# Kernel optimization log

Measured on AMD Instinct MI355X. Metric: run time of the kernel, lower is better.

The kernel has to match this reference:

```python
import jax, jax.numpy as jnp
import numpy as np

B, T, I, H, NL, HORIZON, NQ = 256, 512, 64, 512, 2, 30, 3
MEDIAN_IDX = 1  # quantiles.index(0.5)


def _lstm_cell(xt, h, c, Wih, Whh, b):
    # PyTorch gate order: i, f, g, o
    g = xt @ Wih.T + h @ Whh.T + b
    i, f, gg, o = jnp.split(g, 4, axis=-1)
    c_new = jax.nn.sigmoid(f) * c + jax.nn.sigmoid(i) * jnp.tanh(gg)
    h_new = jax.nn.sigmoid(o) * jnp.tanh(c_new)
    return h_new, c_new


def _run_lstm_layer(xs, Wih, Whh, b):
    # xs: [T, B, in]; zero initial state (torch default)
    batch = xs.shape[1]
    hidden = Whh.shape[1]
    h0 = jnp.zeros((batch, hidden), xs.dtype)

    def step(carry, xt):
        h, c = carry
        h, c = _lstm_cell(xt, h, c, Wih, Whh, b)
        return (h, c), h

    (hT, cT), hs = jax.lax.scan(step, (h0, h0), xs)
    return hs, hT, cT


def setup_inputs() -> dict:
    key = jax.random.key(0)
    ks = jax.random.split(key, 24)
    k = 1.0 / np.sqrt(H)

    def u(kk, shape):
        return jax.random.uniform(kk, shape, jnp.float32, -k, k)

    inp = {
        "x": jax.random.normal(ks[0], (B, T, I), jnp.float32),
        # encoder layer 0 (input I) and layer 1 (input H)
        "enc_Wih0": u(ks[1], (4 * H, I)),
        "enc_Whh0": u(ks[2], (4 * H, H)),
        "enc_bih0": u(ks[3], (4 * H,)),
        "enc_bhh0": u(ks[4], (4 * H,)),
        "enc_Wih1": u(ks[5], (4 * H, H)),
        "enc_Whh1": u(ks[6], (4 * H, H)),
        "enc_bih1": u(ks[7], (4 * H,)),
        "enc_bhh1": u(ks[8], (4 * H,)),
        # decoder layer 0 (input H+1) and layer 1 (input H)
        "dec_Wih0": u(ks[9], (4 * H, H + 1)),
        "dec_Whh0": u(ks[10], (4 * H, H)),
        "dec_bih0": u(ks[11], (4 * H,)),
        "dec_bhh0": u(ks[12], (4 * H,)),
        "dec_Wih1": u(ks[13], (4 * H, H)),
        "dec_Whh1": u(ks[14], (4 * H, H)),
        "dec_bih1": u(ks[15], (4 * H,)),
        "dec_bhh1": u(ks[16], (4 * H,)),
        # attention: W [H,H] (no bias), V [H] (Linear(H,1) weight)
        "attn_W": u(ks[17], (H, H)),
        "attn_v": u(ks[18], (H,)),
        # output projection [NQ, H] + bias
        "out_W": u(ks[19], (NQ, H)),
        "out_b": u(ks[20], (NQ,)),
    }
    return inp


def reference(x, enc_Wih0, enc_Whh0, enc_bih0, enc_bhh0,
              enc_Wih1, enc_Whh1, enc_bih1, enc_bhh1,
              dec_Wih0, dec_Whh0, dec_bih0, dec_bhh0,
              dec_Wih1, dec_Whh1, dec_bih1, dec_bhh1,
              attn_W, attn_v, out_W, out_b):
    # ---- encoder: 2-layer LSTM over time (eval mode: no dropout) ----
    xs = jnp.transpose(x, (1, 0, 2))  # [T, B, I]
    hs0, _, _ = _run_lstm_layer(xs, enc_Wih0, enc_Whh0, enc_bih0 + enc_bhh0)
    hs1, h_last, c_last = _run_lstm_layer(hs0, enc_Wih1, enc_Whh1, enc_bih1 + enc_bhh1)
    encoder_outputs = jnp.transpose(hs1, (1, 0, 2))  # [B, T, H]

    # precompute W(encoder_outputs) once (same math as per-step recompute)
    enc_proj = jnp.einsum('bth,gh->btg', encoder_outputs, attn_W)  # [B, T, H]

    b_dec0 = dec_bih0 + dec_bhh0
    b_dec1 = dec_bih1 + dec_bhh1

    dec_input0 = x[:, -1, 0:1]  # [B, 1]

    def step(carry, _):
        h, c, inp = carry
        # Bahdanau attention
        dec_proj = h @ attn_W.T  # [B, H]
        energies = jnp.einsum('bth,h->bt', jnp.tanh(enc_proj + dec_proj[:, None, :]), attn_v)
        attn = jax.nn.softmax(energies, axis=1)  # [B, T]
        ctx = jnp.einsum('bt,bth->bh', attn, encoder_outputs)  # [B, H]
        # decoder LSTM, 1 timestep; both layers restart from the SAME (h, c)
        # (the module repeats the last layer's state across layers each step)
        x0 = jnp.concatenate([inp, ctx], axis=1)  # [B, H+1]
        h0, c0 = _lstm_cell(x0, h, c, dec_Wih0, dec_Whh0, b_dec0)
        h1, c1 = _lstm_cell(h0, h, c, dec_Wih1, dec_Whh1, b_dec1)
        out = h1 @ out_W.T + out_b  # [B, NQ]
        new_inp = out[:, MEDIAN_IDX:MEDIAN_IDX + 1]  # feed back median quantile
        return (h1, c1, new_inp), out

    _, preds = jax.lax.scan(step, (h_last, c_last, dec_input0), None, length=HORIZON)
    return jnp.transpose(preds, (1, 0, 2))  # [B, HORIZON, NQ]
```

## Files before the change

### kernel.cpp

```cpp
#include <hip/hip_runtime.h>


typedef _Float16 half_t;
typedef __attribute__((ext_vector_type(8)))  _Float16 f16x8;
typedef __attribute__((ext_vector_type(16))) float    f32x16;

#define MFMA(a,b,c) __builtin_amdgcn_mfma_f32_32x32x16_f16((a),(b),(c),0,0,0)
#define CBAR()      asm volatile("" ::: "memory")
#define AUXC 17

template<int N> __device__ __forceinline__ void waitvm() {
  asm volatile("s_waitcnt vmcnt(%0)" :: "n"(N) : "memory");
}

__device__ __forceinline__ float fsig(float x)  { return 1.0f / (1.0f + __expf(-x)); }
__device__ __forceinline__ float ftanh(float x) { return 1.0f - 2.0f / (1.0f + __expf(2.0f * x)); }

union FU { float f; unsigned u; };
union HU { _Float16 h; unsigned short u; };
__device__ __forceinline__ float ldfa(const float* p) {
  unsigned v = __hip_atomic_load((const unsigned*)p, __ATOMIC_RELAXED, __HIP_MEMORY_SCOPE_AGENT);
  FU c; c.u = v; return c.f;
}
__device__ __forceinline__ void stfa(float* p, float v) {
  FU c; c.f = v;
  __hip_atomic_store((unsigned*)p, c.u, __ATOMIC_RELAXED, __HIP_MEMORY_SCOPE_AGENT);
}
__device__ __forceinline__ void stha(half_t* p, float v) {
  HU c; c.h = (half_t)v;
  __hip_atomic_store((unsigned short*)p, c.u, __ATOMIC_RELAXED, __HIP_MEMORY_SCOPE_AGENT);
}
__device__ __forceinline__ void st64(float* p, float a, float b) {
  FU x, y; x.f = a; y.f = b;
  unsigned long long v = (unsigned long long)x.u | ((unsigned long long)y.u << 32);
  __hip_atomic_store((unsigned long long*)p, v, __ATOMIC_RELAXED, __HIP_MEMORY_SCOPE_AGENT);
}
__device__ __forceinline__ void ld64(const float* p, float& a, float& b) {
  unsigned long long v = __hip_atomic_load((const unsigned long long*)p, __ATOMIC_RELAXED, __HIP_MEMORY_SCOPE_AGENT);
  FU x, y; x.u = (unsigned)v; y.u = (unsigned)(v >> 32); a = x.f; b = y.f;
}

static constexpr size_t O_X16 = 0;
static constexpr size_t O_WL0 = O_X16 + (size_t)512*256*128*2;
static constexpr size_t O_WL1 = O_WL0 + (size_t)2048*640*2;
static constexpr size_t O_WP1 = O_WL1 + (size_t)2048*1024*2;
static constexpr size_t O_WD0 = O_WP1 + (size_t)4672*512*2;
static constexpr size_t O_WD1 = O_WD0 + (size_t)2048*512*2;
static constexpr size_t O_BL0 = O_WD1 + (size_t)2048*512*2;
static constexpr size_t O_BL1 = O_BL0 + 8192;
static constexpr size_t O_BD0 = O_BL1 + 8192;
static constexpr size_t O_BD1 = O_BD0 + 8192;
static constexpr size_t O_W0C = O_BD1 + 8192;
static constexpr size_t O_H0B = O_W0C + 8192;
static constexpr size_t O_H1B = O_H0B + (size_t)2*256*512*2;
static constexpr size_t O_HD1 = O_H1B + (size_t)2*256*512*2;
static constexpr size_t O_H0D = O_HD1 + (size_t)256*512*2;
static constexpr size_t O_CTX = O_H0D + (size_t)256*512*2;
static constexpr size_t O_C0  = O_CTX + (size_t)256*512*2;
static constexpr size_t O_C1  = O_C0  + (size_t)256*512*4;
static constexpr size_t O_INP = O_C1  + (size_t)256*512*4;
static constexpr size_t O_GAT = O_INP + 1024;
static constexpr size_t O_EO  = O_GAT + (size_t)256*4672*4;
static constexpr size_t O_EP  = O_EO  + (size_t)256*512*512*2;
static constexpr size_t WS_NEED = O_EP + (size_t)256*512*512*2;

__device__ __align__(4096) unsigned char g_ws[WS_NEED];
__device__ int g_bar[2048];
__device__ int g_flags[1024];

#define WSH(o) ((half_t*)(g_ws + (o)))
#define WSCH(o) ((const half_t*)(g_ws + (o)))
#define WSF(o) ((float*)(g_ws + (o)))
#define WSCF(o) ((const float*)(g_ws + (o)))
#define BLINE(i) (g_bar + ((size_t)(i) << 5))

__device__ __forceinline__ int gperm(int n) { return (n & 3) * 512 + (n >> 2); }

__device__ __forceinline__ void gbarf(int g, int r, int step) {
  __syncthreads();
  if (threadIdx.x < 64) {
    if (threadIdx.x == 0)
      __hip_atomic_store(&g_flags[(g << 6) + r], step,
                         __ATOMIC_RELAXED, __HIP_MEMORY_SCOPE_AGENT);
    const int* fp = &g_flags[(g << 6) + threadIdx.x];
    for (;;) {
      int v = __hip_atomic_load(fp, __ATOMIC_RELAXED, __HIP_MEMORY_SCOPE_AGENT);
      if (__all(v >= step)) break;
      __builtin_amdgcn_s_sleep(1);
    }
  }
  __syncthreads();
}

__device__ __forceinline__ void gbar_acq(int g, int sub) {
  __syncthreads();
  if (threadIdx.x == 0) {
    int* cnt = BLINE(g * 2 + sub);
    int* mst = BLINE(8 + g);
    int* gs  = BLINE(12 + g * 2 + sub);
    int old = __hip_atomic_load(gs, __ATOMIC_RELAXED, __HIP_MEMORY_SCOPE_AGENT);
    int a = __hip_atomic_fetch_add(cnt, 1, __ATOMIC_ACQ_REL, __HIP_MEMORY_SCOPE_AGENT);
    if (a == 31) {
      __hip_atomic_store(cnt, 0, __ATOMIC_RELAXED, __HIP_MEMORY_SCOPE_AGENT);
      int m = __hip_atomic_fetch_add(mst, 1, __ATOMIC_ACQ_REL, __HIP_MEMORY_SCOPE_AGENT);
      if (m == 1) {
        __hip_atomic_store(mst, 0, __ATOMIC_RELAXED, __HIP_MEMORY_SCOPE_AGENT);
        __hip_atomic_fetch_add(BLINE(12 + g * 2), 1, __ATOMIC_RELEASE, __HIP_MEMORY_SCOPE_AGENT);
        __hip_atomic_fetch_add(BLINE(12 + g * 2 + 1), 1, __ATOMIC_RELEASE, __HIP_MEMORY_SCOPE_AGENT);
      }
    }
    while (__hip_atomic_load(gs, __ATOMIC_RELAXED, __HIP_MEMORY_SCOPE_AGENT) == old)
      __builtin_amdgcn_s_sleep(2);
    (void)__hip_atomic_load(gs, __ATOMIC_ACQUIRE, __HIP_MEMORY_SCOPE_AGENT);
  }
  __syncthreads();
}

struct Seg { const half_t* p; int stride; int row0; };

template<int AXA, int AXB>
__device__ __forceinline__ void stageA(Seg sa, Seg sb, int cSplit, int c,
                                       int lane, int wid, char* dst) {
  bool isA = c < cSplit;
  Seg s = isA ? sa : sb;
  int kb = (isA ? c : (c - cSplit)) * 128;
  const half_t* g = s.p + (size_t)(s.row0 + (lane & 31)) * s.stride
                        + kb + (wid << 4) + ((lane >> 5) << 3);
  if (isA) {
    __builtin_amdgcn_global_load_lds(
        (const __attribute__((address_space(1))) unsigned int*)g,
        (__attribute__((address_space(3))) unsigned int*)dst, 16, 0, AXA);
    __builtin_amdgcn_global_load_lds(
        (const __attribute__((address_space(1))) unsigned int*)(g + (size_t)32 * s.stride),
        (__attribute__((address_space(3))) unsigned int*)(dst + 1024), 16, 0, AXA);
  } else {
    __builtin_amdgcn_global_load_lds(
        (const __attribute__((address_space(1))) unsigned int*)g,
        (__attribute__((address_space(3))) unsigned int*)dst, 16, 0, AXB);
    __builtin_amdgcn_global_load_lds(
        (const __attribute__((address_space(1))) unsigned int*)(g + (size_t)32 * s.stride),
        (__attribute__((address_space(3))) unsigned int*)(dst + 1024), 16, 0, AXB);
  }
}

template<int C, int NC, int CSPLIT, int AXA, int AXB>
__device__ __forceinline__ void kreg(Seg sa, Seg sb,
                                     const f16x8 (&B0)[8], const f16x8 (&B1)[8],
                                     int lane, int wid, char* asg, f32x16 acc[2][2]) {
  if constexpr (C < NC) {
    constexpr int rem = NC - 1 - C;
    waitvm<2 * (rem < 3 ? rem : 3)>();
    char* ab = asg + (size_t)(((C & 3) * 8 + wid)) * 2048 + lane * 16;
    f16x8 a0 = *(const f16x8*)ab;
    f16x8 a1 = *(const f16x8*)(ab + 1024);
    acc[0][0] = MFMA(a0, B0[C], acc[0][0]);
    acc[0][1] = MFMA(a0, B1[C], acc[0][1]);
    acc[1][0] = MFMA(a1, B0[C], acc[1][0]);
    acc[1][1] = MFMA(a1, B1[C], acc[1][1]);
    if constexpr (C + 4 < NC)
      stageA<AXA, AXB>(sa, sb, CSPLIT, C + 4, lane, wid,
                       asg + (size_t)((((C + 4) & 3) * 8 + wid)) * 2048);
    CBAR();
    kreg<C + 1, NC, CSPLIT, AXA, AXB>(sa, sb, B0, B1, lane, wid, asg, acc);
  }
}

template<int NC, int CSPLIT, int AXA, int AXB>
__device__ __forceinline__ void gemm_regB(Seg sa, Seg sb,
                                          const f16x8 (&B0)[8], const f16x8 (&B1)[8],
                                          int lane, int wid, char* asg, f32x16 acc[2][2]) {
  #pragma unroll
  for (int c = 0; c < (NC < 4 ? NC : 4); c++) {
    stageA<AXA, AXB>(sa, sb, CSPLIT, c, lane, wid, asg + (size_t)((c & 3) * 8 + wid) * 2048);
    CBAR();
  }
  kreg<0, NC, CSPLIT, AXA, AXB>(sa, sb, B0, B1, lane, wid, asg, acc);
}

template<int C, int NC>
__device__ __forceinline__ void kks(int lane, int wid, char* asg, f32x16 acc[2][2],
                                    f16x8 (&b0)[4], f16x8 (&b1)[4]) {
  if constexpr (C < NC) {
    waitvm<4 * (NC - 1 - C)>();
    char* ab = asg + (size_t)(C * 8 + wid) * 2048 + lane * 16;
    f16x8 a0 = *(const f16x8*)ab;
    f16x8 a1 = *(const f16x8*)(ab + 1024);
    acc[0][0] = MFMA(a0, b0[C], acc[0][0]);
    acc[0][1] = MFMA(a0, b1[C], acc[0][1]);
    acc[1][0] = MFMA(a1, b0[C], acc[1][0]);
    acc[1][1] = MFMA(a1, b1[C], acc[1][1]);
    CBAR();
    kks<C + 1, NC>(lane, wid, asg, acc, b0, b1);
  }
}

template<int NC, int AXA, int AXB>
__device__ __forceinline__ void gemm_ks(Seg sa, Seg sb, int cSplit, const half_t* Wt,
                                        int lane, int wid, char* asg, f32x16 acc[2][2]) {
  const half_t* wb = Wt + (wid << 1) * 512 + lane * 8;
  f16x8 b0[4], b1[4];
  #pragma unroll
  for (int c = 0; c < NC; c++) {
    stageA<AXA, AXB>(sa, sb, cSplit, c, lane, wid, asg + (size_t)(c * 8 + wid) * 2048);
    CBAR();
    b0[c] = *(const f16x8*)(wb + (size_t)c * 8192);
    b1[c] = *(const f16x8*)(wb + (size_t)c * 8192 + 512);
    CBAR();
  }
  kks<0, NC>(lane, wid, asg, acc, b0, b1);
}

__device__ __forceinline__ void acc_wr(float* dst, int lane, f32x16 acc[2][2]) {
  #pragma unroll
  for (int t = 0; t < 4; t++) {
    f32x16 a = acc[t >> 1][t & 1];
    #pragma unroll
    for (int r4 = 0; r4 < 4; r4++)
      *(float4*)(dst + ((t * 4 + r4) * 64 + lane) * 4) =
          make_float4(a[r4*4], a[r4*4+1], a[r4*4+2], a[r4*4+3]);
  }
}
__device__ __forceinline__ void acc_add(const float* src, int lane, f32x16 acc[2][2]) {
  #pragma unroll
  for (int t = 0; t < 4; t++) {
    #pragma unroll
    for (int r4 = 0; r4 < 4; r4++) {
      float4 v = *(const float4*)(src + ((t * 4 + r4) * 64 + lane) * 4);
      acc[t>>1][t&1][r4*4]   += v.x;
      acc[t>>1][t&1][r4*4+1] += v.y;
      acc[t>>1][t&1][r4*4+2] += v.z;
      acc[t>>1][t&1][r4*4+3] += v.w;
    }
  }
}
__device__ __forceinline__ void reduce8(f32x16 acc[2][2], float* red, int lane, int wid) {
  if (wid >= 4) acc_wr(red + (size_t)(wid - 4) * 4096, lane, acc);
  __syncthreads();
  if (wid < 4) acc_add(red + (size_t)wid * 4096, lane, acc);
  if (wid == 2 || wid == 3) acc_wr(red + (size_t)wid * 4096, lane, acc);
  __syncthreads();
  if (wid < 2) {
    acc_add(red + (size_t)(wid + 2) * 4096, lane, acc);
    float* zone = red + 8192 + (size_t)wid * 4096;
    #pragma unroll
    for (int ms = 0; ms < 2; ms++)
      #pragma unroll
      for (int ns = 0; ns < 2; ns++)
        #pragma unroll
        for (int rr = 0; rr < 16; rr++) {
          int row = ms * 32 + (rr & 3) + ((rr >> 2) << 3) + ((lane >> 5) << 2);
          zone[row * 64 + ns * 32 + (lane & 31)] = acc[ms][ns][rr];
        }
  }
  __syncthreads();
}
__device__ __forceinline__ float4 rsum4(const float* red, int row, int col) {
  float4 a = *(const float4*)&red[8192 + row * 64 + col];
  float4 b = *(const float4*)&red[12288 + row * 64 + col];
  return make_float4(a.x + b.x, a.y + b.y, a.z + b.z, a.w + b.w);
}

__global__ void __launch_bounds__(512, 2) kmain(const float* __restrict__ attn_v,
                                                const float* __restrict__ out_b,
                                                float* __restrict__ out) {
  __shared__ __align__(16) char asg[65536];
  __shared__ float red[16384];

  const half_t* x16 = WSCH(O_X16);
  const half_t* wL0 = WSCH(O_WL0);
  const half_t* wL1 = WSCH(O_WL1);
  const half_t* wP1 = WSCH(O_WP1);
  const half_t* wD0 = WSCH(O_WD0);
  const half_t* wD1 = WSCH(O_WD1);
  half_t* h0bB = WSH(O_H0B);
  half_t* h1bB = WSH(O_H1B);
  half_t* hd1  = WSH(O_HD1);
  half_t* h0d  = WSH(O_H0D);
  half_t* ctx  = WSH(O_CTX);
  half_t* eo   = WSH(O_EO);
  half_t* ep   = WSH(O_EP);
  float* c1 = WSF(O_C1);
  float* inp = WSF(O_INP);
  float* gates = WSF(O_GAT);

  const int tid = threadIdx.x;
  const int wid = tid >> 6;
  const int lane = tid & 63;
  const int g = blockIdx.x & 3;
  const int r = blockIdx.x >> 2;
  const int sub = r & 1;
  const int m0 = g << 6;
  const f32x16 zv = {0,0,0,0,0,0,0,0,0,0,0,0,0,0,0,0};
  int bstep = 0;

  {
    const bool isL1 = r >= 32;
    const int n0 = (r & 31) << 6;

    const half_t* wbase = isL1 ? (wL1 + (size_t)(n0 >> 6) * (8 * 8192))
                               : (wL0 + (size_t)(n0 >> 6) * (5 * 8192));
    const half_t* wb = wbase + (wid << 1) * 512 + lane * 8;
    const int ncB = isL1 ? 8 : 5;
    f16x8 B0[8], B1[8];
    #pragma unroll
    for (int c = 0; c < 8; c++) {
      if (c < ncB) {
        B0[c] = *(const f16x8*)(wb + (size_t)c * 8192);
        B1[c] = *(const f16x8*)(wb + (size_t)c * 8192 + 512);
      }
    }
    const int eu = tid & 15;
    const int ebl = tid >> 4;
    const float* bias = isL1 ? WSCF(O_BL1) : WSCF(O_BL0);
    float4 breg = *(const float4*)&bias[n0 + eu * 4];
    float creg0 = 0.f, creg1 = 0.f;

    for (int s = 0; s <= 512; s++) {
      const bool active = isL1 ? (s > 0) : (s < 512);
      if (active) {
        const half_t* h0r = h0bB + (size_t)((s + 1) & 1) * (256 * 512);
        f32x16 acc[2][2] = {{zv, zv}, {zv, zv}};
        int t;
        if (!isL1) {
          t = s;
          gemm_regB<5, 1, 0, AUXC>(Seg{x16, 128, t * 256 + m0}, Seg{h0r, 512, m0},
                                   B0, B1, lane, wid, asg, acc);
        } else {
          t = s - 1;
          const half_t* h1r = h1bB + (size_t)(s & 1) * (256 * 512);
          gemm_regB<8, 4, AUXC, AUXC>(Seg{h0r, 512, m0}, Seg{h1r, 512, m0},
                                      B0, B1, lane, wid, asg, acc);
        }
        reduce8(acc, red, lane, wid);
        half_t* hb = isL1 ? (h1bB + (size_t)((s - 1) & 1) * (256 * 512))
                          : (h0bB + (size_t)(s & 1) * (256 * 512));
        #pragma unroll
        for (int it = 0; it < 2; it++) {
          int bl = ebl + it * 32;
          float4 g4 = rsum4(red, bl, eu * 4);
          float gi = g4.x + breg.x, gf = g4.y + breg.y;
          float gz = g4.z + breg.z, go = g4.w + breg.w;
          float cold = it ? creg1 : creg0;
          float cn = fsig(gf) * cold + fsig(gi) * ftanh(gz);
          float hn = fsig(go) * ftanh(cn);
          if (it) creg1 = cn; else creg0 = cn;
          int bg = m0 + bl, ug = (n0 >> 2) + eu;
          stha(&hb[bg * 512 + ug], hn);
          if (isL1) eo[((size_t)bg * 512 + t) * 512 + ug] = (half_t)hn;
        }
      }
      gbarf(g, r, ++bstep);
    }

    if (isL1) {
      int ug = (n0 >> 2) + eu;
      c1[(m0 + ebl) * 512 + ug] = creg0;
      c1[(m0 + ebl + 32) * 512 + ug] = creg1;
    }
  }
  gbar_acq(g, sub);

  for (int j = 0; j < 64; j++) {
    const int jj = r * 64 + j;
    const int ml = jj >> 3;
    const int nt = jj & 7;
    const int row0 = (g << 15) + ml * 64;
    f32x16 acc[2][2] = {{zv, zv}, {zv, zv}};
    gemm_ks<4, 0, 0>(Seg{eo, 512, row0}, Seg{eo, 512, row0}, 4,
                     wP1 + (size_t)nt * (4 * 8192), lane, wid, asg, acc);
    reduce8(acc, red, lane, wid);
    {
      int row = tid >> 3, col = (tid & 7) * 8;
      float4 a0 = rsum4(red, row, col);
      float4 a1 = rsum4(red, row, col + 4);
      f16x8 h8;
      h8[0] = (half_t)a0.x; h8[1] = (half_t)a0.y; h8[2] = (half_t)a0.z; h8[3] = (half_t)a0.w;
      h8[4] = (half_t)a1.x; h8[5] = (half_t)a1.y; h8[6] = (half_t)a1.z; h8[7] = (half_t)a1.w;
      *(f16x8*)&ep[(size_t)(row0 + row) * 512 + nt * 64 + col] = h8;
    }
    __syncthreads();
  }
  gbar_acq(g, sub);

  for (int d = 0; d <= 30; d++) {
    const half_t* hs = (d == 0) ? (h1bB + 256 * 512) : hd1;
    for (int jj = r; jj < 73; jj += 64) {
      const int n0p = jj * 64;
      f32x16 acc[2][2] = {{zv, zv}, {zv, zv}};
      gemm_ks<4, AUXC, AUXC>(Seg{hs, 512, m0}, Seg{hs, 512, m0}, 4,
                             wP1 + (size_t)jj * (4 * 8192), lane, wid, asg, acc);
      reduce8(acc, red, lane, wid);
      if (n0p < 4608) {
        #pragma unroll
        for (int it = 0; it < 2; it++) {
          int q = it * 512 + tid;
          int row = q >> 4, col = (q & 15) * 4;
          float4 v4 = rsum4(red, row, col);
          float* dst = &gates[(size_t)(m0 + row) * 4672 + n0p + col];
          st64(dst, v4.x, v4.y);
          st64(dst + 2, v4.z, v4.w);
        }
      } else if (d > 0) {
        if (tid < 64) {
          int bg = m0 + tid;
          float v0 = red[8192 + tid * 64 + 0] + red[12288 + tid * 64 + 0] + out_b[0];
          float v1 = red[8192 + tid * 64 + 1] + red[12288 + tid * 64 + 1] + out_b[1];
          float v2 = red[8192 + tid * 64 + 2] + red[12288 + tid * 64 + 2] + out_b[2];
          out[(size_t)bg * 90 + (d - 1) * 3 + 0] = v0;
          out[(size_t)bg * 90 + (d - 1) * 3 + 1] = v1;
          out[(size_t)bg * 90 + (d - 1) * 3 + 2] = v2;
          stfa(&inp[bg], v1);
        }
      }
      __syncthreads();
    }
    gbarf(g, r, ++bstep);
    if (d == 30) break;

    {
      const int b = m0 + r;
      float* dpb = red;
      float* vb  = red + 512;
      float* eb  = red + 1024;
      float* ab2 = red + 2048;
      float* sc  = red + 2560;
      float* pm  = red + 4096;
      dpb[tid] = ldfa(&gates[(size_t)b * 4672 + tid]);
      vb[tid]  = attn_v[tid];
      __syncthreads();
      float va[8], da[8];
      {
        float4 t0 = *(const float4*)&vb[lane * 8];
        float4 t1 = *(const float4*)&vb[lane * 8 + 4];
        float4 t2 = *(const float4*)&dpb[lane * 8];
        float4 t3 = *(const float4*)&dpb[lane * 8 + 4];
        va[0]=t0.x; va[1]=t0.y; va[2]=t0.z; va[3]=t0.w;
        va[4]=t1.x; va[5]=t1.y; va[6]=t1.z; va[7]=t1.w;
        da[0]=t2.x; da[1]=t2.y; da[2]=t2.z; da[3]=t2.w;
        da[4]=t3.x; da[5]=t3.y; da[6]=t3.z; da[7]=t3.w;
      }
      const half_t* eprow = ep + ((size_t)b << 18) + (size_t)(wid * 64) * 512 + lane * 8;
      for (int tt = 0; tt < 64; tt++) {
        f16x8 e8 = *(const f16x8*)(eprow + (size_t)tt * 512);
        float sum = 0.f;
        #pragma unroll
        for (int jq = 0; jq < 8; jq++)
          sum += va[jq] * ftanh((float)e8[jq] + da[jq]);
        #pragma unroll
        for (int off = 32; off > 0; off >>= 1) sum += __shfl_down(sum, off, 64);
        if (lane == 0) eb[wid * 64 + tt] = sum;
      }
      __syncthreads();
      float e0 = eb[tid];
      float mx = e0;
      #pragma unroll
      for (int off = 32; off > 0; off >>= 1) mx = fmaxf(mx, __shfl_xor(mx, off, 64));
      if (lane == 0) sc[wid] = mx;
      __syncthreads();
      mx = sc[0];
      #pragma unroll
      for (int q = 1; q < 8; q++) mx = fmaxf(mx, sc[q]);
      float x0 = __expf(e0 - mx);
      float ssum = x0;
      #pragma unroll
      for (int off = 32; off > 0; off >>= 1) ssum += __shfl_xor(ssum, off, 64);
      __syncthreads();
      if (lane == 0) sc[8 + wid] = ssum;
      __syncthreads();
      float tot = sc[8];
      #pragma unroll
      for (int q = 1; q < 8; q++) tot += sc[8 + q];
      float inv = 1.f / tot;
      ab2[tid] = x0 * inv;
      __syncthreads();
      float pacc[8] = {0,0,0,0,0,0,0,0};
      const half_t* eow = eo + ((size_t)b << 18) + (size_t)(wid * 64) * 512 + lane * 8;
      for (int tt = 0; tt < 64; tt++) {
        f16x8 h8 = *(const f16x8*)(eow + (size_t)tt * 512);
        float at = ab2[wid * 64 + tt];
        #pragma unroll
        for (int jq = 0; jq < 8; jq++) pacc[jq] += at * (float)h8[jq];
      }
      #pragma unroll
      for (int jq = 0; jq < 8; jq++) pm[wid * 512 + lane * 8 + jq] = pacc[jq];
      __syncthreads();
      float sctx = 0.f;
      #pragma unroll
      for (int w = 0; w < 8; w++) sctx += pm[w * 512 + tid];
      stha(&ctx[(b << 9) + tid], sctx);
    }
    gbarf(g, r, ++bstep);

    if (r < 32) {
      const int n0 = r << 6;
      f32x16 acc[2][2] = {{zv, zv}, {zv, zv}};
      gemm_ks<4, AUXC, AUXC>(Seg{ctx, 512, m0}, Seg{ctx, 512, m0}, 4,
                             wD0 + (size_t)(n0 >> 6) * (4 * 8192), lane, wid, asg, acc);
      reduce8(acc, red, lane, wid);
      const float* bD0 = WSCF(O_BD0);
      const float* w0c = WSCF(O_W0C);
      #pragma unroll
      for (int it = 0; it < 2; it++) {
        int q = it * 512 + tid;
        int u = q & 15, bl = q >> 4;
        int bg = m0 + bl, ug = (n0 >> 2) + u, nl = n0 + u * 4;
        float4 g4 = rsum4(red, bl, u * 4);
        float p0, p1, p2, p3;
        ld64(&gates[(size_t)bg * 4672 + 512 + nl], p0, p1);
        ld64(&gates[(size_t)bg * 4672 + 512 + nl + 2], p2, p3);
        float4 b4 = *(const float4*)&bD0[nl];
        float4 w4 = *(const float4*)&w0c[nl];
        float iv = ldfa(&inp[bg]);
        float gi = g4.x + p0 + b4.x + iv * w4.x;
        float gf = g4.y + p1 + b4.y + iv * w4.y;
        float gz = g4.z + p2 + b4.z + iv * w4.z;
        float go = g4.w + p3 + b4.w + iv * w4.w;
        float cold = c1[bg * 512 + ug];
        float cn = fsig(gf) * cold + fsig(gi) * ftanh(gz);
        stha(&h0d[bg * 512 + ug], fsig(go) * ftanh(cn));
      }
    }
    gbarf(g, r, ++bstep);

    if (r < 32) {
      const int n0 = r << 6;
      f32x16 acc[2][2] = {{zv, zv}, {zv, zv}};
      gemm_ks<4, AUXC, AUXC>(Seg{h0d, 512, m0}, Seg{h0d, 512, m0}, 4,
                             wD1 + (size_t)(n0 >> 6) * (4 * 8192), lane, wid, asg, acc);
      reduce8(acc, red, lane, wid);
      const float* bD1 = WSCF(O_BD1);
      #pragma unroll
      for (int it = 0; it < 2; it++) {
        int q = it * 512 + tid;
        int u = q & 15, bl = q >> 4;
        int bg = m0 + bl, ug = (n0 >> 2) + u, nl = n0 + u * 4;
        float4 g4 = rsum4(red, bl, u * 4);
        float p0, p1, p2, p3;
        ld64(&gates[(size_t)bg * 4672 + 2560 + nl], p0, p1);
        ld64(&gates[(size_t)bg * 4672 + 2560 + nl + 2], p2, p3);
        float4 b4 = *(const float4*)&bD1[nl];
        float gi = g4.x + p0 + b4.x;
        float gf = g4.y + p1 + b4.y;
        float gz = g4.z + p2 + b4.z;
        float go = g4.w + p3 + b4.w;
        float cold = c1[bg * 512 + ug];
        float cn = fsig(gf) * cold + fsig(gi) * ftanh(gz);
        float hn = fsig(go) * ftanh(cn);
        c1[bg * 512 + ug] = cn;
        stha(&hd1[bg * 512 + ug], hn);
      }
    }
    gbarf(g, r, ++bstep);
  }
}

__global__ void kpackB(size_t dstOff, int id, int Ntiles, int NC,
                       const float* s0, const float* s1,
                       const float* s2, const float* s3) {
  half_t* dst = (half_t*)(g_ws + dstOff);
  size_t total = (size_t)Ntiles * NC * 8192;
  size_t i = (size_t)blockIdx.x * 256 + threadIdx.x;
  size_t stride = (size_t)gridDim.x * 256;
  for (size_t e = i; e < total; e += stride) {
    int j = e & 7;
    int l = (e >> 3) & 63;
    int bh = (e >> 9) & 1;
    int w = (e >> 10) & 7;
    int tc = (int)(e >> 13);
    int c = tc % NC;
    int tile = tc / NC;
    int n = tile * 64 + bh * 32 + (l & 31);
    int k = c * 128 + w * 16 + ((l >> 5) << 3) + j;
    float v = 0.f;
    if (id == 0) {
      int pn = gperm(n);
      if (k < 64) v = s0[(size_t)pn * 64 + k];
      else if (k >= 128) v = s1[(size_t)pn * 512 + (k - 128)];
    } else if (id == 1) {
      int pn = gperm(n);
      v = (k < 512) ? s0[(size_t)pn * 512 + k] : s1[(size_t)pn * 512 + (k - 512)];
    } else if (id == 2) {
      if (n < 512) v = s0[((size_t)n << 9) + k];
      else if (n < 2560) v = s1[((size_t)gperm(n - 512) << 9) + k];
      else if (n < 4608) v = s2[((size_t)gperm(n - 2560) << 9) + k];
      else if (n < 4611) v = s3[((size_t)(n - 4608) << 9) + k];
    } else if (id == 3) {
      v = s0[(size_t)gperm(n) * 513 + 1 + k];
    } else {
      v = s0[((size_t)gperm(n) << 9) + k];
    }
    dst[e] = (half_t)v;
  }
}

__global__ void kmisc(const float* ebih0, const float* ebhh0, const float* ebih1, const float* ebhh1,
                      const float* dbih0, const float* dbhh0, const float* dbih1, const float* dbhh1,
                      const float* dWih0, const float* x) {
  float* bL0 = WSF(O_BL0);
  float* bL1 = WSF(O_BL1);
  float* bD0 = WSF(O_BD0);
  float* bD1 = WSF(O_BD1);
  float* w0c = WSF(O_W0C);
  half_t* h0b = WSH(O_H0B);
  half_t* h1b = WSH(O_H1B);
  float* c1 = WSF(O_C1);
  float* inp = WSF(O_INP);
  int i = blockIdx.x * 256 + threadIdx.x, stride = gridDim.x * 256;
  for (int idx = i; idx < 262144; idx += stride) {
    if (idx < 2048) {
      int pn = gperm(idx);
      bL0[idx] = ebih0[pn] + ebhh0[pn];
      bL1[idx] = ebih1[pn] + ebhh1[pn];
      bD0[idx] = dbih0[pn] + dbhh0[pn];
      bD1[idx] = dbih1[pn] + dbhh1[pn];
      w0c[idx] = dWih0[(size_t)pn * 513];
      g_bar[idx] = 0;
    }
    if (idx < 1024) g_flags[idx] = 0;
    if (idx < 256) inp[idx] = x[((size_t)idx * 512 + 511) * 64];
    h0b[idx] = (half_t)0.f;
    h1b[idx] = (half_t)0.f;
    if (idx < 131072) c1[idx] = 0.f;
  }
}

__global__ void kx16(const float* x) {
  half_t* dst = WSH(O_X16);
  size_t i = (size_t)blockIdx.x * 256 + threadIdx.x;
  size_t stride = (size_t)gridDim.x * 256;
  for (size_t e = i; e < (size_t)512 * 256 * 128; e += stride) {
    int t = (int)(e >> 15);
    int b = (int)((e >> 7) & 255);
    int ii = (int)(e & 127);
    dst[e] = (ii < 64) ? (half_t)x[((size_t)b * 512 + t) * 64 + ii] : (half_t)0.f;
  }
}

extern "C" void kernel_launch(void* const* d_in, const int* in_sizes, int n_in,
                              void* d_out, int out_size, void* d_ws, size_t ws_size,
                              hipStream_t stream) {
  const float* x     = (const float*)d_in[0];
  const float* eWih0 = (const float*)d_in[1];
  const float* eWhh0 = (const float*)d_in[2];
  const float* ebih0 = (const float*)d_in[3];
  const float* ebhh0 = (const float*)d_in[4];
  const float* eWih1 = (const float*)d_in[5];
  const float* eWhh1 = (const float*)d_in[6];
  const float* ebih1 = (const float*)d_in[7];
  const float* ebhh1 = (const float*)d_in[8];
  const float* dWih0 = (const float*)d_in[9];
  const float* dWhh0 = (const float*)d_in[10];
  const float* dbih0 = (const float*)d_in[11];
  const float* dbhh0 = (const float*)d_in[12];
  const float* dWih1 = (const float*)d_in[13];
  const float* dWhh1 = (const float*)d_in[14];
  const float* dbih1 = (const float*)d_in[15];
  const float* dbhh1 = (const float*)d_in[16];
  const float* attnW = (const float*)d_in[17];
  const float* attnv = (const float*)d_in[18];
  const float* outW  = (const float*)d_in[19];
  const float* outb  = (const float*)d_in[20];
  (void)in_sizes; (void)n_in; (void)out_size; (void)d_ws; (void)ws_size;

  kpackB<<<1024, 256, 0, stream>>>(O_WL0, 0, 32, 5, eWih0, eWhh0, nullptr, nullptr);
  kpackB<<<1024, 256, 0, stream>>>(O_WL1, 1, 32, 8, eWih1, eWhh1, nullptr, nullptr);
  kpackB<<<1024, 256, 0, stream>>>(O_WP1, 2, 73, 4, attnW, dWhh0, dWhh1, outW);
  kpackB<<<1024, 256, 0, stream>>>(O_WD0, 3, 32, 4, dWih0, nullptr, nullptr, nullptr);
  kpackB<<<1024, 256, 0, stream>>>(O_WD1, 4, 32, 4, dWih1, nullptr, nullptr, nullptr);
  kmisc<<<1024, 256, 0, stream>>>(ebih0, ebhh0, ebih1, ebhh1,
                                  dbih0, dbhh0, dbih1, dbhh1, dWih0, x);
  kx16<<<2048, 256, 0, stream>>>(x);

  float* outp = (float*)d_out;
  void* args[] = {(void*)&attnv, (void*)&outb, (void*)&outp};
  hipError_t e = hipLaunchCooperativeKernel((void*)kmain, dim3(256), dim3(512),
                                            args, 0, stream);
  if (e != hipSuccess) {
    kmain<<<dim3(256), dim3(512), 0, stream>>>(attnv, outb, outp);
  }
}
```

Before: 8.513 ms.

## Repartition persistent LSTM kernel into 8 XCC-local groups with fused encoder layers

```diff
diff --git a/kernel.cpp b/kernel.cpp
--- a/kernel.cpp
+++ b/kernel.cpp
@@ -7,7 +7,6 @@
 
 #define MFMA(a,b,c) __builtin_amdgcn_mfma_f32_32x32x16_f16((a),(b),(c),0,0,0)
 #define CBAR()      asm volatile("" ::: "memory")
-#define AUXC 17
 
 template<int N> __device__ __forceinline__ void waitvm() {
   asm volatile("s_waitcnt vmcnt(%0)" :: "n"(N) : "memory");
@@ -18,25 +17,53 @@
 
 union FU { float f; unsigned u; };
 union HU { _Float16 h; unsigned short u; };
+
+template<bool FAST>
 __device__ __forceinline__ float ldfa(const float* p) {
-  unsigned v = __hip_atomic_load((const unsigned*)p, __ATOMIC_RELAXED, __HIP_MEMORY_SCOPE_AGENT);
-  FU c; c.u = v; return c.f;
-}
+  if constexpr (FAST) {
+    float v;
+    asm volatile("global_load_dword %0, %1, off sc0\n\ts_waitcnt vmcnt(0)"
+                 : "=v"(v) : "v"(p) : "memory");
+    return v;
+  } else {
+    unsigned v = __hip_atomic_load((const unsigned*)p, __ATOMIC_RELAXED, __HIP_MEMORY_SCOPE_AGENT);
+    FU c; c.u = v; return c.f;
+  }
+}
+template<bool FAST>
 __device__ __forceinline__ void stfa(float* p, float v) {
   FU c; c.f = v;
-  __hip_atomic_store((unsigned*)p, c.u, __ATOMIC_RELAXED, __HIP_MEMORY_SCOPE_AGENT);
-}
+  if constexpr (FAST)
+    asm volatile("global_store_dword %0, %1, off sc0" :: "v"(p), "v"(c.u) : "memory");
+  else
+    __hip_atomic_store((unsigned*)p, c.u, __ATOMIC_RELAXED, __HIP_MEMORY_SCOPE_AGENT);
+}
+template<bool FAST>
 __device__ __forceinline__ void stha(half_t* p, float v) {
   HU c; c.h = (half_t)v;
-  __hip_atomic_store((unsigned short*)p, c.u, __ATOMIC_RELAXED, __HIP_MEMORY_SCOPE_AGENT);
-}
+  if constexpr (FAST)
+    asm volatile("global_store_short %0, %1, off sc0" :: "v"(p), "v"((unsigned)c.u) : "memory");
+  else
+    __hip_atomic_store((unsigned short*)p, c.u, __ATOMIC_RELAXED, __HIP_MEMORY_SCOPE_AGENT);
+}
+template<bool FAST>
 __device__ __forceinline__ void st64(float* p, float a, float b) {
   FU x, y; x.f = a; y.f = b;
   unsigned long long v = (unsigned long long)x.u | ((unsigned long long)y.u << 32);
-  __hip_atomic_store((unsigned long long*)p, v, __ATOMIC_RELAXED, __HIP_MEMORY_SCOPE_AGENT);
-}
+  if constexpr (FAST)
+    asm volatile("global_store_dwordx2 %0, %1, off sc0" :: "v"(p), "v"(v) : "memory");
+  else
+    __hip_atomic_store((unsigned long long*)p, v, __ATOMIC_RELAXED, __HIP_MEMORY_SCOPE_AGENT);
+}
+template<bool FAST>
 __device__ __forceinline__ void ld64(const float* p, float& a, float& b) {
-  unsigned long long v = __hip_atomic_load((const unsigned long long*)p, __ATOMIC_RELAXED, __HIP_MEMORY_SCOPE_AGENT);
+  unsigned long long v;
+  if constexpr (FAST) {
+    asm volatile("global_load_dwordx2 %0, %1, off sc0\n\ts_waitcnt vmcnt(0)"
+                 : "=v"(v) : "v"(p) : "memory");
+  } else {
+    v = __hip_atomic_load((const unsigned long long*)p, __ATOMIC_RELAXED, __HIP_MEMORY_SCOPE_AGENT);
+  }
   FU x, y; x.u = (unsigned)v; y.u = (unsigned)(v >> 32); a = x.f; b = y.f;
 }
 
@@ -67,6 +94,7 @@
 __device__ __align__(4096) unsigned char g_ws[WS_NEED];
 __device__ int g_bar[2048];
 __device__ int g_flags[1024];
+__device__ int g_xcc[256];
 
 #define WSH(o) ((half_t*)(g_ws + (o)))
 #define WSCH(o) ((const half_t*)(g_ws + (o)))
@@ -80,9 +108,9 @@
   __syncthreads();
   if (threadIdx.x < 64) {
     if (threadIdx.x == 0)
-      __hip_atomic_store(&g_flags[(g << 6) + r], step,
+      __hip_atomic_store(&g_flags[(g << 5) + r], step,
                          __ATOMIC_RELAXED, __HIP_MEMORY_SCOPE_AGENT);
-    const int* fp = &g_flags[(g << 6) + threadIdx.x];
+    const int* fp = &g_flags[(g << 5) + (threadIdx.x & 31)];
     for (;;) {
       int v = __hip_atomic_load(fp, __ATOMIC_RELAXED, __HIP_MEMORY_SCOPE_AGENT);
       if (__all(v >= step)) break;
@@ -92,21 +120,22 @@
   __syncthreads();
 }
 
-__device__ __forceinline__ void gbar_acq(int g, int sub) {
+__device__ __forceinline__ void gbar_acq8() {
   __syncthreads();
   if (threadIdx.x == 0) {
-    int* cnt = BLINE(g * 2 + sub);
-    int* mst = BLINE(8 + g);
-    int* gs  = BLINE(12 + g * 2 + sub);
+    const int g = blockIdx.x & 7;
+    int* cnt = BLINE(g);
+    int* mst = BLINE(8);
+    int* gs  = BLINE(16 + g);
     int old = __hip_atomic_load(gs, __ATOMIC_RELAXED, __HIP_MEMORY_SCOPE_AGENT);
     int a = __hip_atomic_fetch_add(cnt, 1, __ATOMIC_ACQ_REL, __HIP_MEMORY_SCOPE_AGENT);
     if (a == 31) {
       __hip_atomic_store(cnt, 0, __ATOMIC_RELAXED, __HIP_MEMORY_SCOPE_AGENT);
       int m = __hip_atomic_fetch_add(mst, 1, __ATOMIC_ACQ_REL, __HIP_MEMORY_SCOPE_AGENT);
-      if (m == 1) {
+      if (m == 7) {
         __hip_atomic_store(mst, 0, __ATOMIC_RELAXED, __HIP_MEMORY_SCOPE_AGENT);
-        __hip_atomic_fetch_add(BLINE(12 + g * 2), 1, __ATOMIC_RELEASE, __HIP_MEMORY_SCOPE_AGENT);
-        __hip_atomic_fetch_add(BLINE(12 + g * 2 + 1), 1, __ATOMIC_RELEASE, __HIP_MEMORY_SCOPE_AGENT);
+        for (int q = 0; q < 8; q++)
+          __hip_atomic_fetch_add(BLINE(16 + q), 1, __ATOMIC_RELEASE, __HIP_MEMORY_SCOPE_AGENT);
       }
     }
     while (__hip_atomic_load(gs, __ATOMIC_RELAXED, __HIP_MEMORY_SCOPE_AGENT) == old)
@@ -114,6 +143,13 @@
     (void)__hip_atomic_load(gs, __ATOMIC_ACQUIRE, __HIP_MEMORY_SCOPE_AGENT);
   }
   __syncthreads();
+}
+
+template<int AX>
+__device__ __forceinline__ void gld(const half_t* gp, char* lp) {
+  __builtin_amdgcn_global_load_lds(
+      (const __attribute__((address_space(1))) unsigned int*)gp,
+      (__attribute__((address_space(3))) unsigned int*)lp, 16, 0, AX);
 }
 
 struct Seg { const half_t* p; int stride; int row0; };
@@ -124,57 +160,15 @@
   bool isA = c < cSplit;
   Seg s = isA ? sa : sb;
   int kb = (isA ? c : (c - cSplit)) * 128;
-  const half_t* g = s.p + (size_t)(s.row0 + (lane & 31)) * s.stride
-                        + kb + (wid << 4) + ((lane >> 5) << 3);
+  const half_t* gp = s.p + (size_t)(s.row0 + (lane & 31)) * s.stride
+                         + kb + (wid << 4) + ((lane >> 5) << 3);
   if (isA) {
-    __builtin_amdgcn_global_load_lds(
-        (const __attribute__((address_space(1))) unsigned int*)g,
-        (__attribute__((address_space(3))) unsigned int*)dst, 16, 0, AXA);
-    __builtin_amdgcn_global_load_lds(
-        (const __attribute__((address_space(1))) unsigned int*)(g + (size_t)32 * s.stride),
-        (__attribute__((address_space(3))) unsigned int*)(dst + 1024), 16, 0, AXA);
+    gld<AXA>(gp, dst);
+    gld<AXA>(gp + (size_t)32 * s.stride, dst + 1024);
   } else {
-    __builtin_amdgcn_global_load_lds(
-        (const __attribute__((address_space(1))) unsigned int*)g,
-        (__attribute__((address_space(3))) unsigned int*)dst, 16, 0, AXB);
-    __builtin_amdgcn_global_load_lds(
-        (const __attribute__((address_space(1))) unsigned int*)(g + (size_t)32 * s.stride),
-        (__attribute__((address_space(3))) unsigned int*)(dst + 1024), 16, 0, AXB);
-  }
-}
-
-template<int C, int NC, int CSPLIT, int AXA, int AXB>
-__device__ __forceinline__ void kreg(Seg sa, Seg sb,
-                                     const f16x8 (&B0)[8], const f16x8 (&B1)[8],
-                                     int lane, int wid, char* asg, f32x16 acc[2][2]) {
-  if constexpr (C < NC) {
-    constexpr int rem = NC - 1 - C;
-    waitvm<2 * (rem < 3 ? rem : 3)>();
-    char* ab = asg + (size_t)(((C & 3) * 8 + wid)) * 2048 + lane * 16;
-    f16x8 a0 = *(const f16x8*)ab;
-    f16x8 a1 = *(const f16x8*)(ab + 1024);
-    acc[0][0] = MFMA(a0, B0[C], acc[0][0]);
-    acc[0][1] = MFMA(a0, B1[C], acc[0][1]);
-    acc[1][0] = MFMA(a1, B0[C], acc[1][0]);
-    acc[1][1] = MFMA(a1, B1[C], acc[1][1]);
-    if constexpr (C + 4 < NC)
-      stageA<AXA, AXB>(sa, sb, CSPLIT, C + 4, lane, wid,
-                       asg + (size_t)((((C + 4) & 3) * 8 + wid)) * 2048);
-    CBAR();
-    kreg<C + 1, NC, CSPLIT, AXA, AXB>(sa, sb, B0, B1, lane, wid, asg, acc);
-  }
-}
-
-template<int NC, int CSPLIT, int AXA, int AXB>
-__device__ __forceinline__ void gemm_regB(Seg sa, Seg sb,
-                                          const f16x8 (&B0)[8], const f16x8 (&B1)[8],
-                                          int lane, int wid, char* asg, f32x16 acc[2][2]) {
-  #pragma unroll
-  for (int c = 0; c < (NC < 4 ? NC : 4); c++) {
-    stageA<AXA, AXB>(sa, sb, CSPLIT, c, lane, wid, asg + (size_t)((c & 3) * 8 + wid) * 2048);
-    CBAR();
-  }
-  kreg<0, NC, CSPLIT, AXA, AXB>(sa, sb, B0, B1, lane, wid, asg, acc);
+    gld<AXB>(gp, dst);
+    gld<AXB>(gp + (size_t)32 * s.stride, dst + 1024);
+  }
 }
 
 template<int C, int NC>
@@ -208,6 +202,61 @@
     CBAR();
   }
   kks<0, NC>(lane, wid, asg, acc, b0, b1);
+}
+
+template<int C, int NC>
+__device__ __forceinline__ void kks32(char* wslr, f32x16 (&acc)[2][2],
+                                      f16x8 (&b0)[4], f16x8 (&b1)[4]) {
+  if constexpr (C < NC) {
+    waitvm<3 * (NC - 1 - C) + 2>();
+    f16x8 a = *(const f16x8*)(wslr + C * 8192);
+    acc[0][0] = MFMA(a, b0[C], acc[0][0]);
+    acc[0][1] = MFMA(a, b1[C], acc[0][1]);
+    CBAR();
+    kks32<C + 1, NC>(wslr, acc, b0, b1);
+  }
+}
+
+template<int NC, int AX>
+__device__ __forceinline__ void gemm_ks32(const half_t* aP, const half_t* Wt,
+                                          int lane, int wid, char* asg, f32x16 (&acc)[2][2]) {
+  char* wsl = asg + wid * 1024;
+  const half_t* wb = Wt + (wid << 1) * 512 + lane * 8;
+  f16x8 b0[4], b1[4];
+  #pragma unroll
+  for (int c = 0; c < NC; c++) {
+    gld<AX>(aP + c * 128, wsl + c * 8192);
+    CBAR();
+    b0[c] = *(const f16x8*)(wb + (size_t)c * 8192);
+    b1[c] = *(const f16x8*)(wb + (size_t)c * 8192 + 512);
+    CBAR();
+  }
+  kks32<0, NC>(wsl + lane * 16, acc, b0, b1);
+}
+
+template<int C>
+__device__ __forceinline__ void encL0(const char* wslr, const f16x8 (&B0)[5],
+                                      const f16x8 (&B1)[5], f32x16 (&acc)[2][2]) {
+  if constexpr (C < 5) {
+    waitvm<8 - C>();
+    f16x8 a = *(const f16x8*)(wslr + C * 8192);
+    acc[0][0] = MFMA(a, B0[C], acc[0][0]);
+    acc[0][1] = MFMA(a, B1[C], acc[0][1]);
+    CBAR();
+    encL0<C + 1>(wslr, B0, B1, acc);
+  }
+}
+template<int C>
+__device__ __forceinline__ void encL1(const char* wslr, const f16x8 (&B0)[8],
+                                      const f16x8 (&B1)[8], f32x16 (&acc)[2][2]) {
+  if constexpr (C < 8) {
+    if constexpr (C >= 4) waitvm<7 - C>();
+    f16x8 a = *(const f16x8*)(wslr + (C + 1) * 8192);
+    acc[1][0] = MFMA(a, B0[C], acc[1][0]);
+    acc[1][1] = MFMA(a, B1[C], acc[1][1]);
+    CBAR();
+    encL1<C + 1>(wslr, B0, B1, acc);
+  }
 }
 
 __device__ __forceinline__ void acc_wr(float* dst, int lane, f32x16 acc[2][2]) {
@@ -260,11 +309,12 @@
   return make_float4(a.x + b.x, a.y + b.y, a.z + b.z, a.w + b.w);
 }
 
-__global__ void __launch_bounds__(512, 2) kmain(const float* __restrict__ attn_v,
-                                                const float* __restrict__ out_b,
-                                                float* __restrict__ out) {
-  __shared__ __align__(16) char asg[65536];
-  __shared__ float red[16384];
+template<bool FAST>
+__device__ __noinline__ void run_all(int g, int r, const float* attn_v,
+                                     const float* out_b, float* out,
+                                     char* asg, float* red) {
+  constexpr int AXH = FAST ? 1 : 17;
+  constexpr size_t PP = (size_t)256 * 512;
 
   const half_t* x16 = WSCH(O_X16);
   const half_t* wL0 = WSCH(O_WL0);
@@ -286,85 +336,80 @@
   const int tid = threadIdx.x;
   const int wid = tid >> 6;
   const int lane = tid & 63;
-  const int g = blockIdx.x & 3;
-  const int r = blockIdx.x >> 2;
-  const int sub = r & 1;
-  const int m0 = g << 6;
+  const int m0 = g << 5;
   const f32x16 zv = {0,0,0,0,0,0,0,0,0,0,0,0,0,0,0,0};
   int bstep = 0;
 
+  const int koff = (wid << 4) + ((lane >> 5) << 3);
+  const size_t aofs = (size_t)(m0 + (lane & 31)) * 512 + koff;
+  const size_t xofs = (size_t)(m0 + (lane & 31)) * 128 + koff;
+  char* wsl = asg + wid * 1024;
+  const char* wslr = wsl + lane * 16;
+
   {
-    const bool isL1 = r >= 32;
-    const int n0 = (r & 31) << 6;
-
-    const half_t* wbase = isL1 ? (wL1 + (size_t)(n0 >> 6) * (8 * 8192))
-                               : (wL0 + (size_t)(n0 >> 6) * (5 * 8192));
-    const half_t* wb = wbase + (wid << 1) * 512 + lane * 8;
-    const int ncB = isL1 ? 8 : 5;
-    f16x8 B0[8], B1[8];
+    const int n0 = r << 6;
+    const half_t* wb0 = wL0 + (size_t)r * (5 * 8192) + (wid << 1) * 512 + lane * 8;
+    const half_t* wb1 = wL1 + (size_t)r * (8 * 8192) + (wid << 1) * 512 + lane * 8;
+    f16x8 B0L0[5], B1L0[5], B0L1[8], B1L1[8];
+    #pragma unroll
+    for (int c = 0; c < 5; c++) {
+      B0L0[c] = *(const f16x8*)(wb0 + (size_t)c * 8192);
+      B1L0[c] = *(const f16x8*)(wb0 + (size_t)c * 8192 + 512);
+    }
     #pragma unroll
     for (int c = 0; c < 8; c++) {
-      if (c < ncB) {
-        B0[c] = *(const f16x8*)(wb + (size_t)c * 8192);
-        B1[c] = *(const f16x8*)(wb + (size_t)c * 8192 + 512);
+      B0L1[c] = *(const f16x8*)(wb1 + (size_t)c * 8192);
+      B1L1[c] = *(const f16x8*)(wb1 + (size_t)c * 8192 + 512);
+    }
+    const int eu = tid & 15, ebl = tid >> 4;
+    const float4 breg0 = *(const float4*)&(WSCF(O_BL0))[n0 + eu * 4];
+    const float4 breg1 = *(const float4*)&(WSCF(O_BL1))[n0 + eu * 4];
+    const int bg = m0 + ebl, ug = (r << 4) + eu;
+    float creg0 = 0.f, creg1 = 0.f;
+
+    for (int s = 0; s <= 512; s++) {
+      {
+        const int tc = s < 512 ? s : 511;
+        const half_t* xp  = x16 + (((size_t)tc) << 15) + xofs;
+        const half_t* h0p = h0bB + (size_t)((s + 1) & 1) * PP + aofs;
+        const half_t* h1p = h1bB + (size_t)(s & 1) * PP + aofs;
+        gld<0>(xp, wsl);
+        #pragma unroll
+        for (int c = 0; c < 4; c++) gld<AXH>(h0p + c * 128, wsl + (c + 1) * 8192);
+        #pragma unroll
+        for (int c = 0; c < 4; c++) gld<AXH>(h1p + c * 128, wsl + (c + 5) * 8192);
+        CBAR();
       }
-    }
-    const int eu = tid & 15;
-    const int ebl = tid >> 4;
-    const float* bias = isL1 ? WSCF(O_BL1) : WSCF(O_BL0);
-    float4 breg = *(const float4*)&bias[n0 + eu * 4];
-    float creg0 = 0.f, creg1 = 0.f;
-
-    for (int s = 0; s <= 512; s++) {
-      const bool active = isL1 ? (s > 0) : (s < 512);
-      if (active) {
-        const half_t* h0r = h0bB + (size_t)((s + 1) & 1) * (256 * 512);
-        f32x16 acc[2][2] = {{zv, zv}, {zv, zv}};
-        int t;
-        if (!isL1) {
-          t = s;
-          gemm_regB<5, 1, 0, AUXC>(Seg{x16, 128, t * 256 + m0}, Seg{h0r, 512, m0},
-                                   B0, B1, lane, wid, asg, acc);
-        } else {
-          t = s - 1;
-          const half_t* h1r = h1bB + (size_t)(s & 1) * (256 * 512);
-          gemm_regB<8, 4, AUXC, AUXC>(Seg{h0r, 512, m0}, Seg{h1r, 512, m0},
-                                      B0, B1, lane, wid, asg, acc);
-        }
-        reduce8(acc, red, lane, wid);
-        half_t* hb = isL1 ? (h1bB + (size_t)((s - 1) & 1) * (256 * 512))
-                          : (h0bB + (size_t)(s & 1) * (256 * 512));
-        #pragma unroll
-        for (int it = 0; it < 2; it++) {
-          int bl = ebl + it * 32;
-          float4 g4 = rsum4(red, bl, eu * 4);
-          float gi = g4.x + breg.x, gf = g4.y + breg.y;
-          float gz = g4.z + breg.z, go = g4.w + breg.w;
-          float cold = it ? creg1 : creg0;
-          float cn = fsig(gf) * cold + fsig(gi) * ftanh(gz);
-          float hn = fsig(go) * ftanh(cn);
-          if (it) creg1 = cn; else creg0 = cn;
-          int bg = m0 + bl, ug = (n0 >> 2) + eu;
-          stha(&hb[bg * 512 + ug], hn);
-          if (isL1) eo[((size_t)bg * 512 + t) * 512 + ug] = (half_t)hn;
-        }
+      f32x16 acc[2][2] = {{zv, zv}, {zv, zv}};
+      encL0<0>(wslr, B0L0, B1L0, acc);
+      encL1<0>(wslr, B0L1, B1L1, acc);
+      reduce8(acc, red, lane, wid);
+      if (s < 512) {
+        float4 g4 = rsum4(red, ebl, eu * 4);
+        float cn = fsig(g4.y + breg0.y) * creg0 + fsig(g4.x + breg0.x) * ftanh(g4.z + breg0.z);
+        float hn = fsig(g4.w + breg0.w) * ftanh(cn);
+        creg0 = cn;
+        stha<FAST>(&h0bB[(size_t)(s & 1) * PP + (size_t)bg * 512 + ug], hn);
+      }
+      if (s > 0) {
+        float4 g4 = rsum4(red, ebl + 32, eu * 4);
+        float cn = fsig(g4.y + breg1.y) * creg1 + fsig(g4.x + breg1.x) * ftanh(g4.z + breg1.z);
+        float hn = fsig(g4.w + breg1.w) * ftanh(cn);
+        creg1 = cn;
+        stha<FAST>(&h1bB[(size_t)((s + 1) & 1) * PP + (size_t)bg * 512 + ug], hn);
+        eo[((size_t)bg * 512 + (s - 1)) * 512 + ug] = (half_t)hn;
       }
       gbarf(g, r, ++bstep);
     }
-
-    if (isL1) {
-      int ug = (n0 >> 2) + eu;
-      c1[(m0 + ebl) * 512 + ug] = creg0;
-      c1[(m0 + ebl + 32) * 512 + ug] = creg1;
-    }
-  }
-  gbar_acq(g, sub);
+    c1[(size_t)bg * 512 + ug] = creg1;
+  }
+  gbar_acq8();
 
   for (int j = 0; j < 64; j++) {
-    const int jj = r * 64 + j;
+    const int jj = (r << 6) + j;
     const int ml = jj >> 3;
     const int nt = jj & 7;
-    const int row0 = (g << 15) + ml * 64;
+    const int row0 = (g << 14) + ml * 64;
     f32x16 acc[2][2] = {{zv, zv}, {zv, zv}};
     gemm_ks<4, 0, 0>(Seg{eo, 512, row0}, Seg{eo, 512, row0}, 4,
                      wP1 + (size_t)nt * (4 * 8192), lane, wid, asg, acc);
@@ -380,28 +425,24 @@
     }
     __syncthreads();
   }
-  gbar_acq(g, sub);
+  gbar_acq8();
 
   for (int d = 0; d <= 30; d++) {
-    const half_t* hs = (d == 0) ? (h1bB + 256 * 512) : hd1;
-    for (int jj = r; jj < 73; jj += 64) {
-      const int n0p = jj * 64;
+    const half_t* hs = (d == 0) ? (h1bB + PP) : hd1;
+
+    for (int jj = r; jj < 73; jj += 32) {
+      if (d == 30 && jj != 72) continue;
       f32x16 acc[2][2] = {{zv, zv}, {zv, zv}};
-      gemm_ks<4, AUXC, AUXC>(Seg{hs, 512, m0}, Seg{hs, 512, m0}, 4,
-                             wP1 + (size_t)jj * (4 * 8192), lane, wid, asg, acc);
+      gemm_ks32<4, AXH>(hs + aofs, wP1 + (size_t)jj * (4 * 8192), lane, wid, asg, acc);
       reduce8(acc, red, lane, wid);
-      if (n0p < 4608) {
-        #pragma unroll
-        for (int it = 0; it < 2; it++) {
-          int q = it * 512 + tid;
-          int row = q >> 4, col = (q & 15) * 4;
-          float4 v4 = rsum4(red, row, col);
-          float* dst = &gates[(size_t)(m0 + row) * 4672 + n0p + col];
-          st64(dst, v4.x, v4.y);
-          st64(dst + 2, v4.z, v4.w);
-        }
+      if (jj < 72) {
+        int row = tid >> 4, col = (tid & 15) * 4;
+        float4 v4 = rsum4(red, row, col);
+        float* dst = &gates[(size_t)(m0 + row) * 4672 + jj * 64 + col];
+        st64<FAST>(dst, v4.x, v4.y);
+        st64<FAST>(dst + 2, v4.z, v4.w);
       } else if (d > 0) {
-        if (tid < 64) {
+        if (tid < 32) {
           int bg = m0 + tid;
           float v0 = red[8192 + tid * 64 + 0] + red[12288 + tid * 64 + 0] + out_b[0];
           float v1 = red[8192 + tid * 64 + 1] + red[12288 + tid * 64 + 1] + out_b[1];
@@ -409,7 +450,7 @@
           out[(size_t)bg * 90 + (d - 1) * 3 + 0] = v0;
           out[(size_t)bg * 90 + (d - 1) * 3 + 1] = v1;
           out[(size_t)bg * 90 + (d - 1) * 3 + 2] = v2;
-          stfa(&inp[bg], v1);
+          stfa<FAST>(&inp[bg], v1);
         }
       }
       __syncthreads();
@@ -425,7 +466,7 @@
       float* ab2 = red + 2048;
       float* sc  = red + 2560;
       float* pm  = red + 4096;
-      dpb[tid] = ldfa(&gates[(size_t)b * 4672 + tid]);
+      dpb[tid] = ldfa<FAST>(&gates[(size_t)b * 4672 + tid]);
       vb[tid]  = attn_v[tid];
       __syncthreads();
       float va[8], da[8];
@@ -487,71 +528,89 @@
       float sctx = 0.f;
       #pragma unroll
       for (int w = 0; w < 8; w++) sctx += pm[w * 512 + tid];
-      stha(&ctx[(b << 9) + tid], sctx);
+      stha<FAST>(&ctx[((size_t)b << 9) + tid], sctx);
     }
     gbarf(g, r, ++bstep);
 
-    if (r < 32) {
-      const int n0 = r << 6;
+    {
       f32x16 acc[2][2] = {{zv, zv}, {zv, zv}};
-      gemm_ks<4, AUXC, AUXC>(Seg{ctx, 512, m0}, Seg{ctx, 512, m0}, 4,
-                             wD0 + (size_t)(n0 >> 6) * (4 * 8192), lane, wid, asg, acc);
+      gemm_ks32<4, AXH>(ctx + aofs, wD0 + (size_t)r * (4 * 8192), lane, wid, asg, acc);
       reduce8(acc, red, lane, wid);
       const float* bD0 = WSCF(O_BD0);
       const float* w0c = WSCF(O_W0C);
-      #pragma unroll
-      for (int it = 0; it < 2; it++) {
-        int q = it * 512 + tid;
-        int u = q & 15, bl = q >> 4;
-        int bg = m0 + bl, ug = (n0 >> 2) + u, nl = n0 + u * 4;
-        float4 g4 = rsum4(red, bl, u * 4);
-        float p0, p1, p2, p3;
-        ld64(&gates[(size_t)bg * 4672 + 512 + nl], p0, p1);
-        ld64(&gates[(size_t)bg * 4672 + 512 + nl + 2], p2, p3);
-        float4 b4 = *(const float4*)&bD0[nl];
-        float4 w4 = *(const float4*)&w0c[nl];
-        float iv = ldfa(&inp[bg]);
-        float gi = g4.x + p0 + b4.x + iv * w4.x;
-        float gf = g4.y + p1 + b4.y + iv * w4.y;
-        float gz = g4.z + p2 + b4.z + iv * w4.z;
-        float go = g4.w + p3 + b4.w + iv * w4.w;
-        float cold = c1[bg * 512 + ug];
-        float cn = fsig(gf) * cold + fsig(gi) * ftanh(gz);
-        stha(&h0d[bg * 512 + ug], fsig(go) * ftanh(cn));
-      }
+      int u = tid & 15, bl = tid >> 4;
+      int bg = m0 + bl, ug = (r << 4) + u, nl = (r << 6) + u * 4;
+      float4 g4 = rsum4(red, bl, u * 4);
+      float p0, p1, p2, p3;
+      ld64<FAST>(&gates[(size_t)bg * 4672 + 512 + nl], p0, p1);
+      ld64<FAST>(&gates[(size_t)bg * 4672 + 512 + nl + 2], p2, p3);
+      float4 b4 = *(const float4*)&bD0[nl];
+      float4 w4 = *(const float4*)&w0c[nl];
+      float iv = ldfa<FAST>(&inp[bg]);
+      float gi = g4.x + p0 + b4.x + iv * w4.x;
+      float gf = g4.y + p1 + b4.y + iv * w4.y;
+      float gz = g4.z + p2 + b4.z + iv * w4.z;
+      float go = g4.w + p3 + b4.w + iv * w4.w;
+      float cold = c1[(size_t)bg * 512 + ug];
+      float cn = fsig(gf) * cold + fsig(gi) * ftanh(gz);
+      stha<FAST>(&h0d[(size_t)bg * 512 + ug], fsig(go) * ftanh(cn));
     }
     gbarf(g, r, ++bstep);
 
-    if (r < 32) {
-      const int n0 = r << 6;
+    {
       f32x16 acc[2][2] = {{zv, zv}, {zv, zv}};
-      gemm_ks<4, AUXC, AUXC>(Seg{h0d, 512, m0}, Seg{h0d, 512, m0}, 4,
-                             wD1 + (size_t)(n0 >> 6) * (4 * 8192), lane, wid, asg, acc);
+      gemm_ks32<4, AXH>(h0d + aofs, wD1 + (size_t)r * (4 * 8192), lane, wid, asg, acc);
       reduce8(acc, red, lane, wid);
       const float* bD1 = WSCF(O_BD1);
-      #pragma unroll
-      for (int it = 0; it < 2; it++) {
-        int q = it * 512 + tid;
-        int u = q & 15, bl = q >> 4;
-        int bg = m0 + bl, ug = (n0 >> 2) + u, nl = n0 + u * 4;
-        float4 g4 = rsum4(red, bl, u * 4);
-        float p0, p1, p2, p3;
-        ld64(&gates[(size_t)bg * 4672 + 2560 + nl], p0, p1);
-        ld64(&gates[(size_t)bg * 4672 + 2560 + nl + 2], p2, p3);
-        float4 b4 = *(const float4*)&bD1[nl];
-        float gi = g4.x + p0 + b4.x;
-        float gf = g4.y + p1 + b4.y;
-        float gz = g4.z + p2 + b4.z;
-        float go = g4.w + p3 + b4.w;
-        float cold = c1[bg * 512 + ug];
-        float cn = fsig(gf) * cold + fsig(gi) * ftanh(gz);
-        float hn = fsig(go) * ftanh(cn);
-        c1[bg * 512 + ug] = cn;
-        stha(&hd1[bg * 512 + ug], hn);
-      }
+      int u = tid & 15, bl = tid >> 4;
+      int bg = m0 + bl, ug = (r << 4) + u, nl = (r << 6) + u * 4;
+      float4 g4 = rsum4(red, bl, u * 4);
+      float p0, p1, p2, p3;
+      ld64<FAST>(&gates[(size_t)bg * 4672 + 2560 + nl], p0, p1);
+      ld64<FAST>(&gates[(size_t)bg * 4672 + 2560 + nl + 2], p2, p3);
+      float4 b4 = *(const float4*)&bD1[nl];
+      float gi = g4.x + p0 + b4.x;
+      float gf = g4.y + p1 + b4.y;
+      float gz = g4.z + p2 + b4.z;
+      float go = g4.w + p3 + b4.w;
+      float cold = c1[(size_t)bg * 512 + ug];
+      float cn = fsig(gf) * cold + fsig(gi) * ftanh(gz);
+      float hn = fsig(go) * ftanh(cn);
+      c1[(size_t)bg * 512 + ug] = cn;
+      stha<FAST>(&hd1[(size_t)bg * 512 + ug], hn);
     }
     gbarf(g, r, ++bstep);
   }
+}
+
+__global__ void __launch_bounds__(512, 2) kmain(const float* __restrict__ attn_v,
+                                                const float* __restrict__ out_b,
+                                                float* __restrict__ out) {
+  __shared__ __align__(16) char asg[73728];
+  __shared__ float red[16384];
+  __shared__ int smode;
+
+  const int g = blockIdx.x & 7;
+  const int r = blockIdx.x >> 3;
+
+  int xcc = 0;
+  asm volatile("s_getreg_b32 %0, hwreg(HW_REG_XCC_ID)" : "=s"(xcc));
+  if (threadIdx.x == 0)
+    __hip_atomic_store(&g_xcc[blockIdx.x], xcc + 1,
+                       __ATOMIC_RELAXED, __HIP_MEMORY_SCOPE_AGENT);
+  gbar_acq8();
+  if (threadIdx.x < 64) {
+    int p = __hip_atomic_load(&g_xcc[((threadIdx.x & 31) << 3) | g],
+                              __ATOMIC_RELAXED, __HIP_MEMORY_SCOPE_AGENT);
+    int q = __hip_atomic_load(&g_xcc[((threadIdx.x & 31) << 3) | (g ^ 1)],
+                              __ATOMIC_RELAXED, __HIP_MEMORY_SCOPE_AGENT);
+    int p0 = __builtin_amdgcn_readfirstlane(p);
+    int ok = (__all(p == p0) && !__all(q == p0)) ? 1 : 0;
+    if (threadIdx.x == 0) smode = ok;
+  }
+  __syncthreads();
+  if (smode) run_all<true>(g, r, attn_v, out_b, out, asg, red);
+  else       run_all<false>(g, r, attn_v, out_b, out, asg, red);
 }
 
 __global__ void kpackB(size_t dstOff, int id, int Ntiles, int NC,
@@ -617,7 +676,7 @@
       g_bar[idx] = 0;
     }
     if (idx < 1024) g_flags[idx] = 0;
-    if (idx < 256) inp[idx] = x[((size_t)idx * 512 + 511) * 64];
+    if (idx < 256) { inp[idx] = x[((size_t)idx * 512 + 511) * 64]; g_xcc[idx] = 0; }
     h0b[idx] = (half_t)0.f;
     h1b[idx] = (half_t)0.f;
     if (idx < 131072) c1[idx] = 0.f;
```

Result: faster. 6.893 ms (-19.0%).
